# Performance work log

Hardware: AMD Instinct MI355X
Metric: run time of the kernel (lower is better)

Reference implementation:

```python
import jax, jax.numpy as jnp
import numpy as np

B, F, H, D, TE, CE = 16384, 1024, 64, 256, 4, 4

def setup_inputs() -> dict:
    key = jax.random.key(0)
    ks = iter(jax.random.split(key, 40))
    s = 0.02
    mk = lambda shape: jax.random.normal(next(ks), shape, jnp.float32) * s
    inp = {
        'x_A': jax.random.normal(next(ks), (B, F), jnp.float32),
        'x_S': jax.random.normal(next(ks), (B, F), jnp.float32),
        'x_B': jax.random.normal(next(ks), (B, F), jnp.float32),
        # stacked per-expert weights for the three expert groups (A, Shared, B)
        'W1A': mk((TE, F, H)), 'b1A': mk((TE, H)), 'W2A': mk((TE, H, D)), 'b2A': mk((TE, D)),
        'W1S': mk((CE, F, H)), 'b1S': mk((CE, H)), 'W2S': mk((CE, H, D)), 'b2S': mk((CE, D)),
        'W1B': mk((TE, F, H)), 'b1B': mk((TE, H)), 'W2B': mk((TE, H, D)), 'b2B': mk((TE, D)),
        # gate weights
        'WgA': mk((F, TE + CE)), 'bgA': mk((TE + CE,)),
        'WgB': mk((F, TE + CE)), 'bgB': mk((TE + CE,)),
        'WgS': mk((F, 2 * TE + CE)), 'bgS': mk((2 * TE + CE,)),
    }
    return inp

def _expert_group(x, W1, b1, W2, b2):
    # x: [B,F], W1: [E,F,H] -> [B,E,H]; W2: [E,H,D] -> [B,E,D]
    h = jax.nn.relu(jnp.einsum('bf,efh->beh', x, W1) + b1)  # dropout p=0 -> identity
    return jax.nn.relu(jnp.einsum('beh,ehd->bed', h, W2) + b2)

def reference(x_A, x_S, x_B,
              W1A, b1A, W2A, b2A,
              W1S, b1S, W2S, b2S,
              W1B, b1B, W2B, b2B,
              WgA, bgA, WgB, bgB, WgS, bgS):
    EA = _expert_group(x_A, W1A, b1A, W2A, b2A)  # [B,TE,D]
    ES = _expert_group(x_S, W1S, b1S, W2S, b2S)  # [B,CE,D]
    EB = _expert_group(x_B, W1B, b1B, W2B, b2B)  # [B,TE,D]
    gA = jax.nn.softmax(x_A @ WgA + bgA, axis=1)  # [B,TE+CE]
    gS = jax.nn.softmax(x_S @ WgS + bgS, axis=1)  # [B,2TE+CE]
    gB = jax.nn.softmax(x_B @ WgB + bgB, axis=1)  # [B,TE+CE]
    outA = jnp.einsum('bed,be->bd', jnp.concatenate([EA, ES], axis=1), gA)
    outS = jnp.einsum('bed,be->bd', jnp.concatenate([EA, ES, EB], axis=1), gS)
    outB = jnp.einsum('bed,be->bd', jnp.concatenate([EB, ES], axis=1), gB)
    return (outA, outS, outB)
```

## Files before the change

kernel.cpp:

```cpp
#include <hip/hip_runtime.h>


#define BB 16384
#define FF 1024

typedef _Float16 f16;
typedef __fp16 h16x2 __attribute__((ext_vector_type(2)));
typedef _Float16 f16x8 __attribute__((ext_vector_type(8)));
typedef float f32x4 __attribute__((ext_vector_type(4)));

__device__ __forceinline__ void load_lds16(const void* g, void* l) {
    __builtin_amdgcn_global_load_lds(
        (const __attribute__((address_space(1))) unsigned int*)g,
        (__attribute__((address_space(3))) unsigned int*)l, 16, 0, 0);
}

__device__ __forceinline__ f16x8 pack8(float4 lo, float4 hi) {
    union { f16x8 v; h16x2 p[4]; } u;
    u.p[0] = __builtin_amdgcn_cvt_pkrtz(lo.x, lo.y);
    u.p[1] = __builtin_amdgcn_cvt_pkrtz(lo.z, lo.w);
    u.p[2] = __builtin_amdgcn_cvt_pkrtz(hi.x, hi.y);
    u.p[3] = __builtin_amdgcn_cvt_pkrtz(hi.z, hi.w);
    return u.v;
}

__global__ __launch_bounds__(256) void pack_kernel(
    const float* __restrict__ W1A, const float* __restrict__ W1S, const float* __restrict__ W1B,
    const float* __restrict__ W2A, const float* __restrict__ W2S, const float* __restrict__ W2B,
    const float* __restrict__ WgA, const float* __restrict__ WgS, const float* __restrict__ WgB,
    f16* __restrict__ Wp, f16* __restrict__ W2T, f16* __restrict__ Gp)
{
    int idx = blockIdx.x * 256 + threadIdx.x;
    if (idx < 786432) {
        int g = idx / 262144, rem = idx % 262144;
        int c = rem >> 10, k = rem & 1023;
        const float* W1 = (g == 0) ? W1A : ((g == 1) ? W1S : W1B);
        Wp[idx] = (f16)W1[((c >> 6) << 16) + k * 64 + (c & 63)];
    } else if (idx < 983040) {
        int j = idx - 786432;
        int g = j / 65536, rem = j % 65536;
        int e = rem >> 14, rr = rem & 16383;
        int d = rr >> 6, hh = rr & 63;
        const float* W2 = (g == 0) ? W2A : ((g == 1) ? W2S : W2B);
        W2T[j] = (f16)W2[e * 16384 + hh * 256 + d];
    } else {
        int j = idx - 983040;
        int g = j / 16384, rem = j % 16384;
        int c = rem >> 10, k = rem & 1023;
        int ng = (g == 1) ? 12 : 8;
        const float* Wg = (g == 0) ? WgA : ((g == 1) ? WgS : WgB);
        Gp[j] = (c < ng) ? (f16)Wg[k * ng + c] : (f16)0.0f;
    }
}

__global__ __launch_bounds__(512, 2) void fused_kernel(
    const float* __restrict__ xA, const float* __restrict__ xS, const float* __restrict__ xB,
    const float* __restrict__ b1A, const float* __restrict__ b1S, const float* __restrict__ b1B,
    const float* __restrict__ bgA, const float* __restrict__ bgS, const float* __restrict__ bgB,
    const float* __restrict__ b2A, const float* __restrict__ b2S, const float* __restrict__ b2B,
    const f16* __restrict__ Wp,
    const f16* __restrict__ Gp,
    const f16* __restrict__ W2T,
    float* __restrict__ out)
{
    extern __shared__ char smem[];
    f16*   hls   = (f16*)smem;
    char*  stage = smem + 98304;
    float* Xs    = (float*)stage;
    f16*   Ws    = (f16*)(stage + 24576);
    f16*   W2s   = (f16*)stage;
    float* b2s   = (float*)(stage + 32768);
    float* gsh   = (float*)(stage + 45056);
    f16*   Gs    = (f16*)(smem + 157696);

    const int tid  = threadIdx.x;
    const int lane = tid & 63;
    const int w    = tid >> 6;
    const int lrow = lane & 15;
    const int quad = lane >> 4;
    const int row0 = blockIdx.x * 64;

    const int wm = (w >> 2) * 32;
    const int wn = (w & 3) * 64;
    const int rblk = (w & 3) * 16;
    const int wn2  = (w >> 2) * 64;

    const bool gate_wave = ((w & 3) == 0);

    float b1vA[4], b1vS[4], b1vB[4];
#pragma unroll
    for (int j = 0; j < 4; ++j) {
        int c = wn + j * 16 + lrow;
        b1vA[j] = b1A[c]; b1vS[j] = b1S[c]; b1vB[j] = b1B[c];
    }
    float bgv0 = (lrow < 8)  ? bgA[lrow] : 0.0f;
    float bgv1 = (lrow < 12) ? bgS[lrow] : 0.0f;
    float bgv2 = (lrow < 8)  ? bgB[lrow] : 0.0f;

    auto stage_x = [&](int t) {
        int g = t >> 5, k0 = (t & 31) * 32;
        const float* xg = (g == 0) ? xA : ((g == 1) ? xS : xB);
        int s = tid;
        int m = s >> 3, slot = s & 7;
        int seg = slot ^ (m & 7);
        load_lds16(xg + (size_t)(row0 + m) * FF + k0 + seg * 4,
                   Xs + (size_t)(t % 3) * 2048 + s * 4);
    };
    auto stage_w = [&](int t) {
        int g = t >> 5, k0 = (t & 31) * 32;
        const f16* wg = Wp + (size_t)g * 262144;
#pragma unroll
        for (int r = 0; r < 2; ++r) {
            int s = r * 512 + tid;
            int m = s >> 2, slot = s & 3;
            int seg = slot ^ ((m >> 1) & 3);
            load_lds16(wg + (size_t)m * FF + k0 + seg * 8,
                       Ws + (size_t)(t & 1) * 8192 + s * 8);
        }
    };
    auto stage_g = [&](int t) {
        int g = t >> 5, k0 = (t & 31) * 32;
        load_lds16(Gp + (size_t)g * 16384 + (size_t)(lane >> 2) * 1024 + k0 + (lane & 3) * 8,
                   Gs + (size_t)(t & 1) * 512 + lane * 8);
    };

    f32x4 acc[2][4] = {};
    f32x4 gacc[2] = {};
    f32x4 gsvA[2], gsvS[2], gsvB[2];

    auto h_write = [&](int g, const float (&bv)[4]) {
        f16* hb = hls + g * 16384;
#pragma unroll
        for (int j = 0; j < 4; ++j) {
            int col = wn + j * 16 + lrow;
            float bias = bv[j];
#pragma unroll
            for (int i = 0; i < 2; ++i)
#pragma unroll
                for (int r = 0; r < 4; ++r) {
                    int row = wm + i * 16 + quad * 4 + r;
                    float v = fmaxf(acc[i][j][r] + bias, 0.0f);
                    hb[row * 256 + (col ^ ((row & 7) << 3))] = (f16)v;
                }
        }
    };

    stage_x(0);
    __builtin_amdgcn_sched_barrier(0);
    stage_w(0);
    __builtin_amdgcn_sched_barrier(0);
    stage_g(0);
    __builtin_amdgcn_sched_barrier(0);
    stage_x(1);
    __builtin_amdgcn_sched_barrier(0);

    for (int t = 0; t < 96; ++t) {
        int t1 = t + 1;
        int t2 = t + 2;
        if (t < 95) {
            stage_w(t1);
            __builtin_amdgcn_sched_barrier(0);
            stage_g(t1);
            __builtin_amdgcn_sched_barrier(0);
        }
        if (t < 94) {
            stage_x(t2);
            __builtin_amdgcn_sched_barrier(0);
        }
        if (t < 94)      { asm volatile("s_waitcnt vmcnt(5)" ::: "memory"); }
        else if (t == 94){ asm volatile("s_waitcnt vmcnt(4)" ::: "memory"); }
        else             { asm volatile("s_waitcnt vmcnt(0)" ::: "memory"); }
        __builtin_amdgcn_sched_barrier(0);
        __builtin_amdgcn_s_barrier();
        __builtin_amdgcn_sched_barrier(0);

        {
            const float* xb = Xs + (t % 3) * 2048;
            const f16* wb = Ws + (t & 1) * 8192;
            f16x8 af[2], bfr[4];
#pragma unroll
            for (int i = 0; i < 2; ++i) {
                int m = wm + i * 16 + lrow;
                const float* rp = xb + m * 32;
                int s0 = (2 * quad) ^ (m & 7);
                float4 lo = *(const float4*)(rp + s0 * 4);
                float4 hi = *(const float4*)(rp + (s0 ^ 1) * 4);
                af[i] = pack8(lo, hi);
            }
#pragma unroll
            for (int j = 0; j < 4; ++j) {
                int n = wn + j * 16 + lrow;
                int slot = quad ^ ((n >> 1) & 3);
                bfr[j] = *(const f16x8*)(wb + n * 32 + slot * 8);
            }
#pragma unroll
            for (int i = 0; i < 2; ++i)
#pragma unroll
                for (int j = 0; j < 4; ++j)
                    acc[i][j] = __builtin_amdgcn_mfma_f32_16x16x32_f16(af[i], bfr[j], acc[i][j], 0, 0, 0);
            if (gate_wave) {
                f16x8 gb = *(const f16x8*)(Gs + (t & 1) * 512 + lrow * 32 + quad * 8);
#pragma unroll
                for (int i = 0; i < 2; ++i)
                    gacc[i] = __builtin_amdgcn_mfma_f32_16x16x32_f16(af[i], gb, gacc[i], 0, 0, 0);
            }
        }

        if ((t & 31) == 31) {
            int g = t >> 5;
            if (g == 0)      { h_write(0, b1vA); if (gate_wave) { gsvA[0] = gacc[0]; gsvA[1] = gacc[1]; } }
            else if (g == 1) { h_write(1, b1vS); if (gate_wave) { gsvS[0] = gacc[0]; gsvS[1] = gacc[1]; } }
            else             { h_write(2, b1vB); if (gate_wave) { gsvB[0] = gacc[0]; gsvB[1] = gacc[1]; } }
#pragma unroll
            for (int i = 0; i < 2; ++i) {
#pragma unroll
                for (int j = 0; j < 4; ++j) acc[i][j] = (f32x4){0.f, 0.f, 0.f, 0.f};
                gacc[i] = (f32x4){0.f, 0.f, 0.f, 0.f};
            }
        }

        asm volatile("s_waitcnt lgkmcnt(0)" ::: "memory");
        __builtin_amdgcn_sched_barrier(0);
        __builtin_amdgcn_s_barrier();
        __builtin_amdgcn_sched_barrier(0);
    }

    auto stage_w2 = [&](int c, int buf) {
        int p = c >> 1, dh = c & 1;
        int gi = p >> 2, e = p & 3;
        const f16* w2 = W2T + (size_t)(gi * 4 + e) * 16384 + (size_t)dh * 8192;
#pragma unroll
        for (int r = 0; r < 2; ++r) {
            int s = r * 512 + tid;
            int m = s >> 3, slot = s & 7;
            int seg = slot ^ (m & 7);
            load_lds16(w2 + (size_t)m * 64 + seg * 8,
                       W2s + (size_t)buf * 8192 + s * 8);
        }
    };

    {
        const float* s1 = (tid < 256) ? (b2A + tid * 4) : (b2S + (tid - 256) * 4);
        load_lds16(s1, b2s + tid * 4);
        __builtin_amdgcn_sched_barrier(0);
        if (tid < 256) load_lds16(b2B + tid * 4, b2s + 2048 + tid * 4);
        __builtin_amdgcn_sched_barrier(0);
    }
    stage_w2(0, 0);
    __builtin_amdgcn_sched_barrier(0);

    if (gate_wave) {
        auto softmax_store = [&](const f32x4 (&gsv)[2], float bgc, int ng, int goff) {
            int c = lrow;
            bool valid = (c < ng);
#pragma unroll
            for (int i = 0; i < 2; ++i)
#pragma unroll
                for (int r = 0; r < 4; ++r) {
                    int row = wm + i * 16 + quad * 4 + r;
                    float logit = valid ? (gsv[i][r] + bgc) : -1e30f;
                    float mx = logit;
#pragma unroll
                    for (int m = 1; m < 16; m <<= 1) mx = fmaxf(mx, __shfl_xor(mx, m, 16));
                    float ev = valid ? __expf(logit - mx) : 0.0f;
                    float sum = ev;
#pragma unroll
                    for (int m = 1; m < 16; m <<= 1) sum += __shfl_xor(sum, m, 16);
                    if (valid) gsh[row * 28 + goff + c] = ev / sum;
                }
        };
        softmax_store(gsvA, bgv0, 8, 0);
        softmax_store(gsvS, bgv1, 12, 8);
        softmax_store(gsvB, bgv2, 8, 20);
    }
    asm volatile("s_waitcnt vmcnt(2) lgkmcnt(0)" ::: "memory");
    __builtin_amdgcn_sched_barrier(0);
    __builtin_amdgcn_s_barrier();
    __builtin_amdgcn_sched_barrier(0);

    f32x4 oA[2][4] = {}, oS[2][4] = {}, oB[2][4] = {};

    for (int p = 0; p < 12; ++p) {
        int gi = p >> 2, e = p & 3;
#pragma unroll
        for (int dh = 0; dh < 2; ++dh) {
            int c = p * 2 + dh;
            if (c < 23) {
                stage_w2(c + 1, dh ^ 1);
                __builtin_amdgcn_sched_barrier(0);
                asm volatile("s_waitcnt vmcnt(2)" ::: "memory");
            } else {
                asm volatile("s_waitcnt vmcnt(0)" ::: "memory");
            }
            __builtin_amdgcn_sched_barrier(0);
            __builtin_amdgcn_s_barrier();
            __builtin_amdgcn_sched_barrier(0);

            float bias[4];
#pragma unroll
            for (int j = 0; j < 4; ++j)
                bias[j] = b2s[gi * 1024 + e * 256 + dh * 128 + wn2 + j * 16 + lrow];

            const f16* wb = W2s + dh * 8192;
            f32x4 eacc[4] = {};
#pragma unroll
            for (int kk = 0; kk < 2; ++kk) {
                int row = rblk + lrow;
                int u = (kk * 32 + quad * 8) ^ ((row & 7) << 3);
                f16x8 af = *(const f16x8*)(hls + gi * 16384 + row * 256 + e * 64 + u);
                f16x8 bfr[4];
#pragma unroll
                for (int j = 0; j < 4; ++j) {
                    int n = wn2 + j * 16 + lrow;
                    int slot = (kk * 4 + quad) ^ (n & 7);
                    bfr[j] = *(const f16x8*)(wb + n * 64 + slot * 8);
                }
#pragma unroll
                for (int j = 0; j < 4; ++j)
                    eacc[j] = __builtin_amdgcn_mfma_f32_16x16x32_f16(af, bfr[j], eacc[j], 0, 0, 0);
            }

#pragma unroll
            for (int r = 0; r < 4; ++r) {
                int row = rblk + quad * 4 + r;
                float ga = 0.f, gs = 0.f, gb = 0.f;
                if (gi == 0)      { ga = gsh[row * 28 + e];      gs = gsh[row * 28 + 8 + e]; }
                else if (gi == 1) { ga = gsh[row * 28 + 4 + e];  gs = gsh[row * 28 + 12 + e]; gb = gsh[row * 28 + 24 + e]; }
                else              { gs = gsh[row * 28 + 16 + e]; gb = gsh[row * 28 + 20 + e]; }
#pragma unroll
                for (int j = 0; j < 4; ++j) {
                    float v = fmaxf(eacc[j][r] + bias[j], 0.0f);
                    if (gi == 0)      { oA[dh][j][r] += ga * v; oS[dh][j][r] += gs * v; }
                    else if (gi == 1) { oA[dh][j][r] += ga * v; oS[dh][j][r] += gs * v; oB[dh][j][r] += gb * v; }
                    else              { oS[dh][j][r] += gs * v; oB[dh][j][r] += gb * v; }
                }
            }

            asm volatile("s_waitcnt lgkmcnt(0)" ::: "memory");
            __builtin_amdgcn_sched_barrier(0);
            __builtin_amdgcn_s_barrier();
            __builtin_amdgcn_sched_barrier(0);
        }
    }

#pragma unroll
    for (int dh = 0; dh < 2; ++dh)
#pragma unroll
        for (int j = 0; j < 4; ++j) {
            int d = dh * 128 + wn2 + j * 16 + lrow;
#pragma unroll
            for (int r = 0; r < 4; ++r) {
                int row = row0 + rblk + quad * 4 + r;
                out[((size_t)0 * BB + row) * 256 + d] = oA[dh][j][r];
                out[((size_t)1 * BB + row) * 256 + d] = oS[dh][j][r];
                out[((size_t)2 * BB + row) * 256 + d] = oB[dh][j][r];
            }
        }
}

extern "C" void kernel_launch(void* const* d_in, const int* in_sizes, int n_in,
                              void* d_out, int out_size, void* d_ws, size_t ws_size,
                              hipStream_t stream)
{
    (void)in_sizes; (void)n_in; (void)out_size; (void)ws_size;

    const float* xA  = (const float*)d_in[0];
    const float* xS  = (const float*)d_in[1];
    const float* xB  = (const float*)d_in[2];
    const float* W1A = (const float*)d_in[3];
    const float* b1A = (const float*)d_in[4];
    const float* W2A = (const float*)d_in[5];
    const float* b2A = (const float*)d_in[6];
    const float* W1S = (const float*)d_in[7];
    const float* b1S = (const float*)d_in[8];
    const float* W2S = (const float*)d_in[9];
    const float* b2S = (const float*)d_in[10];
    const float* W1B = (const float*)d_in[11];
    const float* b1B = (const float*)d_in[12];
    const float* W2B = (const float*)d_in[13];
    const float* b2B = (const float*)d_in[14];
    const float* WgA = (const float*)d_in[15];
    const float* bgA = (const float*)d_in[16];
    const float* WgB = (const float*)d_in[17];
    const float* bgB = (const float*)d_in[18];
    const float* WgS = (const float*)d_in[19];
    const float* bgS = (const float*)d_in[20];

    char* ws = (char*)d_ws;
    f16* Wp  = (f16*)(ws);
    f16* W2T = (f16*)(ws + 0x180000);
    f16* Gp  = (f16*)(ws + 0x1E0000);

    pack_kernel<<<4032, 256, 0, stream>>>(W1A, W1S, W1B, W2A, W2S, W2B,
                                          WgA, WgS, WgB, Wp, W2T, Gp);
    fused_kernel<<<256, 512, 159744, stream>>>(
        xA, xS, xB, b1A, b1S, b1B, bgA, bgS, bgB, b2A, b2S, b2B,
        Wp, Gp, W2T, (float*)d_out);
}
```

Before: 356.1 us.

## Restructure fused MoE kernel: 32-row blocks, register-streamed weights, tiled transpose pack

The pack kernel now transposes W1 and W2 through shared-memory tiles with vectorized loads and stores instead of one scalar gather per element. The fused kernel moves from 64-row, 512-thread blocks to 32-row, 256-thread blocks with 512 blocks, so grid size doubles and LDS per block roughly halves. Layer-1 and layer-2 weight fragments are loaded straight from global memory into double-buffered registers instead of being staged through LDS. Gate MFMAs now run on every wave, and softmax is done per group inside the main loop. This cuts LDS traffic and barrier work per tile but raises register pressure, and each block now re-reads all weights from global memory or cache.

```diff
diff --git a/kernel.cpp b/kernel.cpp
--- a/kernel.cpp
+++ b/kernel.cpp
@@ -6,6 +6,7 @@
 
 typedef _Float16 f16;
 typedef __fp16 h16x2 __attribute__((ext_vector_type(2)));
+typedef _Float16 f16x4 __attribute__((ext_vector_type(4)));
 typedef _Float16 f16x8 __attribute__((ext_vector_type(8)));
 typedef float f32x4 __attribute__((ext_vector_type(4)));
 
@@ -24,36 +25,82 @@
     return u.v;
 }
 
+#define SBAR() __builtin_amdgcn_sched_barrier(0)
+
 __global__ __launch_bounds__(256) void pack_kernel(
     const float* __restrict__ W1A, const float* __restrict__ W1S, const float* __restrict__ W1B,
     const float* __restrict__ W2A, const float* __restrict__ W2S, const float* __restrict__ W2B,
     const float* __restrict__ WgA, const float* __restrict__ WgS, const float* __restrict__ WgB,
     f16* __restrict__ Wp, f16* __restrict__ W2T, f16* __restrict__ Gp)
 {
-    int idx = blockIdx.x * 256 + threadIdx.x;
-    if (idx < 786432) {
-        int g = idx / 262144, rem = idx % 262144;
-        int c = rem >> 10, k = rem & 1023;
+    __shared__ float T[64 * 65];
+    const int b = blockIdx.x, tid = threadIdx.x;
+
+    if (b < 192) {
+        int g = b >> 6, e = (b >> 4) & 3, k0 = (b & 15) * 64;
         const float* W1 = (g == 0) ? W1A : ((g == 1) ? W1S : W1B);
-        Wp[idx] = (f16)W1[((c >> 6) << 16) + k * 64 + (c & 63)];
-    } else if (idx < 983040) {
-        int j = idx - 786432;
-        int g = j / 65536, rem = j % 65536;
-        int e = rem >> 14, rr = rem & 16383;
-        int d = rr >> 6, hh = rr & 63;
+        const float* src = W1 + e * 65536 + k0 * 64;
+#pragma unroll
+        for (int r = 0; r < 4; ++r) {
+            int slot = r * 256 + tid, kr = slot >> 4, h4 = slot & 15;
+            float4 v = *(const float4*)(src + kr * 64 + h4 * 4);
+            T[(h4 * 4 + 0) * 65 + kr] = v.x;
+            T[(h4 * 4 + 1) * 65 + kr] = v.y;
+            T[(h4 * 4 + 2) * 65 + kr] = v.z;
+            T[(h4 * 4 + 3) * 65 + kr] = v.w;
+        }
+        __syncthreads();
+        f16* dst = Wp + g * 262144 + e * 64 * 1024 + k0;
+#pragma unroll
+        for (int r = 0; r < 4; ++r) {
+            int slot = r * 256 + tid, h = slot >> 4, k4 = slot & 15;
+            f16x4 o;
+            o[0] = (f16)T[h * 65 + k4 * 4 + 0];
+            o[1] = (f16)T[h * 65 + k4 * 4 + 1];
+            o[2] = (f16)T[h * 65 + k4 * 4 + 2];
+            o[3] = (f16)T[h * 65 + k4 * 4 + 3];
+            *(f16x4*)(dst + h * 1024 + k4 * 4) = o;
+        }
+    } else if (b < 240) {
+        int bb = b - 192;
+        int g = bb >> 4, e = (bb >> 2) & 3, d0 = (bb & 3) * 64;
         const float* W2 = (g == 0) ? W2A : ((g == 1) ? W2S : W2B);
-        W2T[j] = (f16)W2[e * 16384 + hh * 256 + d];
+        const float* src = W2 + e * 16384 + d0;
+#pragma unroll
+        for (int r = 0; r < 4; ++r) {
+            int slot = r * 256 + tid, hr = slot >> 4, d4 = slot & 15;
+            float4 v = *(const float4*)(src + hr * 256 + d4 * 4);
+            T[(d4 * 4 + 0) * 65 + hr] = v.x;
+            T[(d4 * 4 + 1) * 65 + hr] = v.y;
+            T[(d4 * 4 + 2) * 65 + hr] = v.z;
+            T[(d4 * 4 + 3) * 65 + hr] = v.w;
+        }
+        __syncthreads();
+        f16* dst = W2T + (g * 4 + e) * 16384 + d0 * 64;
+#pragma unroll
+        for (int r = 0; r < 4; ++r) {
+            int slot = r * 256 + tid, dl = slot >> 4, h4 = slot & 15;
+            f16x4 o;
+            o[0] = (f16)T[dl * 65 + h4 * 4 + 0];
+            o[1] = (f16)T[dl * 65 + h4 * 4 + 1];
+            o[2] = (f16)T[dl * 65 + h4 * 4 + 2];
+            o[3] = (f16)T[dl * 65 + h4 * 4 + 3];
+            *(f16x4*)(dst + dl * 64 + h4 * 4) = o;
+        }
     } else {
-        int j = idx - 983040;
-        int g = j / 16384, rem = j % 16384;
-        int c = rem >> 10, k = rem & 1023;
+        int g = b - 240;
         int ng = (g == 1) ? 12 : 8;
         const float* Wg = (g == 0) ? WgA : ((g == 1) ? WgS : WgB);
-        Gp[j] = (c < ng) ? (f16)Wg[k * ng + c] : (f16)0.0f;
+#pragma unroll 4
+        for (int r = 0; r < 64; ++r) {
+            int idx = r * 256 + tid;
+            int c = idx >> 10, k = idx & 1023;
+            Gp[g * 16384 + idx] = (c < ng) ? (f16)Wg[k * ng + c] : (f16)0.0f;
+        }
     }
 }
 
-__global__ __launch_bounds__(512, 2) void fused_kernel(
+__global__ __launch_bounds__(256, 2) void fused_kernel(
     const float* __restrict__ xA, const float* __restrict__ xS, const float* __restrict__ xB,
     const float* __restrict__ b1A, const float* __restrict__ b1S, const float* __restrict__ b1B,
     const float* __restrict__ bgA, const float* __restrict__ bgS, const float* __restrict__ bgB,
@@ -64,28 +111,18 @@
     float* __restrict__ out)
 {
     extern __shared__ char smem[];
-    f16*   hls   = (f16*)smem;
-    char*  stage = smem + 98304;
-    float* Xs    = (float*)stage;
-    f16*   Ws    = (f16*)(stage + 24576);
-    f16*   W2s   = (f16*)stage;
-    float* b2s   = (float*)(stage + 32768);
-    float* gsh   = (float*)(stage + 45056);
-    f16*   Gs    = (f16*)(smem + 157696);
+    f16*   hls = (f16*)smem;
+    float* Xs  = (float*)(smem + 49152);
+    float* b2s = (float*)(smem + 49152);
+    float* gsh = (float*)(smem + 73728);
 
     const int tid  = threadIdx.x;
     const int lane = tid & 63;
     const int w    = tid >> 6;
     const int lrow = lane & 15;
     const int quad = lane >> 4;
-    const int row0 = blockIdx.x * 64;
-
-    const int wm = (w >> 2) * 32;
-    const int wn = (w & 3) * 64;
-    const int rblk = (w & 3) * 16;
-    const int wn2  = (w >> 2) * 64;
-
-    const bool gate_wave = ((w & 3) == 0);
+    const int row0 = blockIdx.x * 32;
+    const int wn   = w * 64;
 
     float b1vA[4], b1vS[4], b1vB[4];
 #pragma unroll
@@ -97,39 +134,60 @@
     float bgv1 = (lrow < 12) ? bgS[lrow] : 0.0f;
     float bgv2 = (lrow < 8)  ? bgB[lrow] : 0.0f;
 
-    auto stage_x = [&](int t) {
-        int g = t >> 5, k0 = (t & 31) * 32;
+    auto stage_x = [&](int tt) {
+        int g = tt >> 4, kb = (tt & 15) * 64;
         const float* xg = (g == 0) ? xA : ((g == 1) ? xS : xB);
-        int s = tid;
-        int m = s >> 3, slot = s & 7;
-        int seg = slot ^ (m & 7);
-        load_lds16(xg + (size_t)(row0 + m) * FF + k0 + seg * 4,
-                   Xs + (size_t)(t % 3) * 2048 + s * 4);
-    };
-    auto stage_w = [&](int t) {
-        int g = t >> 5, k0 = (t & 31) * 32;
-        const f16* wg = Wp + (size_t)g * 262144;
+        float* dstb = Xs + (tt % 3) * 2048;
 #pragma unroll
         for (int r = 0; r < 2; ++r) {
-            int s = r * 512 + tid;
-            int m = s >> 2, slot = s & 3;
-            int seg = slot ^ ((m >> 1) & 3);
-            load_lds16(wg + (size_t)m * FF + k0 + seg * 8,
-                       Ws + (size_t)(t & 1) * 8192 + s * 8);
-        }
-    };
-    auto stage_g = [&](int t) {
-        int g = t >> 5, k0 = (t & 31) * 32;
-        load_lds16(Gp + (size_t)g * 16384 + (size_t)(lane >> 2) * 1024 + k0 + (lane & 3) * 8,
-                   Gs + (size_t)(t & 1) * 512 + lane * 8);
+            int s = r * 256 + tid;
+            int m = s >> 4, slot = s & 15;
+            int seg = slot ^ (m & 15);
+            load_lds16(xg + (size_t)(row0 + m) * FF + kb + seg * 4, dstb + s * 4);
+        }
+    };
+    auto issue_wf = [&](int tt, f16x8 (&wf)[2][4], f16x8 (&gb)[2]) {
+        int g = tt >> 4, kb = (tt & 15) * 64;
+        const f16* ws = Wp + (size_t)g * 262144;
+        const f16* gs = Gp + (size_t)g * 16384;
+#pragma unroll
+        for (int kk = 0; kk < 2; ++kk) {
+#pragma unroll
+            for (int j = 0; j < 4; ++j)
+                wf[kk][j] = *(const f16x8*)(ws + (size_t)(wn + j * 16 + lrow) * 1024 + kb + kk * 32 + quad * 8);
+            gb[kk] = *(const f16x8*)(gs + (size_t)lrow * 1024 + kb + kk * 32 + quad * 8);
+        }
     };
 
     f32x4 acc[2][4] = {};
     f32x4 gacc[2] = {};
-    f32x4 gsvA[2], gsvS[2], gsvB[2];
+
+    auto compute = [&](int t, f16x8 (&wf)[2][4], f16x8 (&gb)[2]) {
+        const float* xb = Xs + (t % 3) * 2048;
+#pragma unroll
+        for (int kk = 0; kk < 2; ++kk) {
+            f16x8 af[2];
+#pragma unroll
+            for (int i = 0; i < 2; ++i) {
+                int m = i * 16 + lrow;
+                int slot = (kk * 8 + quad * 2) ^ (m & 15);
+                const float* rp = xb + m * 64;
+                float4 lo = *(const float4*)(rp + slot * 4);
+                float4 hi = *(const float4*)(rp + (slot ^ 1) * 4);
+                af[i] = pack8(lo, hi);
+            }
+#pragma unroll
+            for (int i = 0; i < 2; ++i) {
+#pragma unroll
+                for (int j = 0; j < 4; ++j)
+                    acc[i][j] = __builtin_amdgcn_mfma_f32_16x16x32_f16(af[i], wf[kk][j], acc[i][j], 0, 0, 0);
+                gacc[i] = __builtin_amdgcn_mfma_f32_16x16x32_f16(af[i], gb[kk], gacc[i], 0, 0, 0);
+            }
+        }
+    };
 
     auto h_write = [&](int g, const float (&bv)[4]) {
-        f16* hb = hls + g * 16384;
+        f16* hb = hls + g * 8192;
 #pragma unroll
         for (int j = 0; j < 4; ++j) {
             int col = wn + j * 16 + lrow;
@@ -138,224 +196,177 @@
             for (int i = 0; i < 2; ++i)
 #pragma unroll
                 for (int r = 0; r < 4; ++r) {
-                    int row = wm + i * 16 + quad * 4 + r;
+                    int row = i * 16 + quad * 4 + r;
                     float v = fmaxf(acc[i][j][r] + bias, 0.0f);
                     hb[row * 256 + (col ^ ((row & 7) << 3))] = (f16)v;
                 }
         }
-    };
-
-    stage_x(0);
-    __builtin_amdgcn_sched_barrier(0);
-    stage_w(0);
-    __builtin_amdgcn_sched_barrier(0);
-    stage_g(0);
-    __builtin_amdgcn_sched_barrier(0);
-    stage_x(1);
-    __builtin_amdgcn_sched_barrier(0);
-
-    for (int t = 0; t < 96; ++t) {
-        int t1 = t + 1;
-        int t2 = t + 2;
-        if (t < 95) {
-            stage_w(t1);
-            __builtin_amdgcn_sched_barrier(0);
-            stage_g(t1);
-            __builtin_amdgcn_sched_barrier(0);
-        }
-        if (t < 94) {
-            stage_x(t2);
-            __builtin_amdgcn_sched_barrier(0);
-        }
-        if (t < 94)      { asm volatile("s_waitcnt vmcnt(5)" ::: "memory"); }
-        else if (t == 94){ asm volatile("s_waitcnt vmcnt(4)" ::: "memory"); }
-        else             { asm volatile("s_waitcnt vmcnt(0)" ::: "memory"); }
-        __builtin_amdgcn_sched_barrier(0);
+#pragma unroll
+        for (int i = 0; i < 2; ++i)
+#pragma unroll
+            for (int j = 0; j < 4; ++j)
+                acc[i][j] = (f32x4){0.f, 0.f, 0.f, 0.f};
+    };
+
+    auto softmax_store = [&](float bgc, int ng, int goff) {
+        bool valid = (lrow < ng);
+#pragma unroll
+        for (int i = 0; i < 2; ++i)
+#pragma unroll
+            for (int r = 0; r < 4; ++r) {
+                int row = i * 16 + quad * 4 + r;
+                float logit = valid ? (gacc[i][r] + bgc) : -1e30f;
+                float mx = logit;
+#pragma unroll
+                for (int m = 1; m < 16; m <<= 1)
+                    mx = fmaxf(mx, __shfl_xor(mx, m, 16));
+                float ev = valid ? __expf(logit - mx) : 0.0f;
+                float sum = ev;
+#pragma unroll
+                for (int m = 1; m < 16; m <<= 1)
+                    sum += __shfl_xor(sum, m, 16);
+                if (valid) gsh[row * 28 + goff + lrow] = ev / sum;
+            }
+    };
+
+    f16x8 wfA[2][4], gbA[2], wfB[2][4], gbB[2];
+
+    stage_x(0); SBAR();
+    issue_wf(0, wfA, gbA); SBAR();
+    stage_x(1); SBAR();
+
+    auto l1_step = [&](int t, f16x8 (&wfC)[2][4], f16x8 (&gbC)[2],
+                       f16x8 (&wfN)[2][4], f16x8 (&gbN)[2]) {
+        issue_wf(t + 1, wfN, gbN);
+        SBAR();
+        asm volatile("s_waitcnt vmcnt(12) lgkmcnt(0)" ::: "memory");
+        SBAR();
         __builtin_amdgcn_s_barrier();
-        __builtin_amdgcn_sched_barrier(0);
-
-        {
-            const float* xb = Xs + (t % 3) * 2048;
-            const f16* wb = Ws + (t & 1) * 8192;
-            f16x8 af[2], bfr[4];
+        SBAR();
+        stage_x(t + 2);
+        SBAR();
+        compute(t, wfC, gbC);
+    };
+
+    for (int tb = 0; tb < 46; tb += 2) {
+        l1_step(tb, wfA, gbA, wfB, gbB);
+        int t1 = tb + 1;
+        l1_step(t1, wfB, gbB, wfA, gbA);
+        if (t1 == 15) {
+            h_write(0, b1vA);
+            if (w == 0) softmax_store(bgv0, 8, 0);
+#pragma unroll
+            for (int i = 0; i < 2; ++i) gacc[i] = (f32x4){0.f, 0.f, 0.f, 0.f};
+        } else if (t1 == 31) {
+            h_write(1, b1vS);
+            if (w == 0) softmax_store(bgv1, 12, 8);
+#pragma unroll
+            for (int i = 0; i < 2; ++i) gacc[i] = (f32x4){0.f, 0.f, 0.f, 0.f};
+        }
+    }
+
+    f16x8 wf2A[2][4], wf2B[2][4];
+    auto issue_wf2 = [&](int p, f16x8 (&wf)[2][4]) {
+        int gi = p >> 2, e = p & 3;
+        const f16* w2 = W2T + (size_t)(gi * 4 + e) * 16384;
+#pragma unroll
+        for (int kk = 0; kk < 2; ++kk)
+#pragma unroll
+            for (int j = 0; j < 4; ++j)
+                wf[kk][j] = *(const f16x8*)(w2 + (size_t)(wn + j * 16 + lrow) * 64 + kk * 32 + quad * 8);
+    };
+
+    issue_wf(47, wfB, gbB);
+    SBAR();
+    asm volatile("s_waitcnt vmcnt(12) lgkmcnt(0)" ::: "memory");
+    SBAR(); __builtin_amdgcn_s_barrier(); SBAR();
+    compute(46, wfA, gbA);
+
+    asm volatile("s_waitcnt vmcnt(0) lgkmcnt(0)" ::: "memory");
+    SBAR(); __builtin_amdgcn_s_barrier(); SBAR();
+#pragma unroll
+    for (int r = 0; r < 3; ++r) {
+        const float* src = (r == 0) ? (b2A + tid * 4) : ((r == 1) ? (b2S + tid * 4) : (b2B + tid * 4));
+        load_lds16(src, b2s + r * 1024 + tid * 4);
+    }
+    SBAR();
+    issue_wf2(0, wf2A);
+    SBAR();
+    compute(47, wfB, gbB);
+    h_write(2, b1vB);
+    if (w == 0) softmax_store(bgv2, 8, 20);
+
+    asm volatile("s_waitcnt vmcnt(8) lgkmcnt(0)" ::: "memory");
+    SBAR(); __builtin_amdgcn_s_barrier(); SBAR();
+
+    f32x4 oA[2][4] = {}, oS[2][4] = {}, oB[2][4] = {};
+
+    auto l2_pair = [&](int p, f16x8 (&wfC)[2][4], f16x8 (&wfN)[2][4]) {
+        if (p < 11) { issue_wf2(p + 1, wfN); }
+        SBAR();
+        if (p < 11) { asm volatile("s_waitcnt vmcnt(8)" ::: "memory"); }
+        else        { asm volatile("s_waitcnt vmcnt(0)" ::: "memory"); }
+        SBAR();
+        const int gi = p >> 2, e = p & 3;
+        f32x4 eacc[2][4] = {};
+#pragma unroll
+        for (int kk = 0; kk < 2; ++kk) {
+            f16x8 af[2];
 #pragma unroll
             for (int i = 0; i < 2; ++i) {
-                int m = wm + i * 16 + lrow;
-                const float* rp = xb + m * 32;
-                int s0 = (2 * quad) ^ (m & 7);
-                float4 lo = *(const float4*)(rp + s0 * 4);
-                float4 hi = *(const float4*)(rp + (s0 ^ 1) * 4);
-                af[i] = pack8(lo, hi);
+                int m = i * 16 + lrow;
+                int col = (e * 64 + kk * 32 + quad * 8) ^ ((m & 7) << 3);
+                af[i] = *(const f16x8*)(hls + gi * 8192 + m * 256 + col);
             }
 #pragma unroll
-            for (int j = 0; j < 4; ++j) {
-                int n = wn + j * 16 + lrow;
-                int slot = quad ^ ((n >> 1) & 3);
-                bfr[j] = *(const f16x8*)(wb + n * 32 + slot * 8);
+            for (int i = 0; i < 2; ++i)
+#pragma unroll
+                for (int j = 0; j < 4; ++j)
+                    eacc[i][j] = __builtin_amdgcn_mfma_f32_16x16x32_f16(af[i], wfC[kk][j], eacc[i][j], 0, 0, 0);
+        }
+#pragma unroll
+        for (int j = 0; j < 4; ++j) {
+            float bias = b2s[gi * 1024 + e * 256 + wn + j * 16 + lrow];
+#pragma unroll
+            for (int i = 0; i < 2; ++i)
+#pragma unroll
+                for (int r = 0; r < 4; ++r) {
+                    int row = i * 16 + quad * 4 + r;
+                    float v = fmaxf(eacc[i][j][r] + bias, 0.0f);
+                    if (gi == 0) {
+                        oA[i][j][r] += gsh[row * 28 + e] * v;
+                        oS[i][j][r] += gsh[row * 28 + 8 + e] * v;
+                    } else if (gi == 1) {
+                        oA[i][j][r] += gsh[row * 28 + 4 + e] * v;
+                        oS[i][j][r] += gsh[row * 28 + 12 + e] * v;
+                        oB[i][j][r] += gsh[row * 28 + 24 + e] * v;
+                    } else {
+                        oS[i][j][r] += gsh[row * 28 + 16 + e] * v;
+                        oB[i][j][r] += gsh[row * 28 + 20 + e] * v;
+                    }
+                }
+        }
+    };
+
+#pragma unroll
+    for (int pp = 0; pp < 6; ++pp) {
+        l2_pair(2 * pp, wf2A, wf2B);
+        l2_pair(2 * pp + 1, wf2B, wf2A);
+    }
+
+#pragma unroll
+    for (int j = 0; j < 4; ++j) {
+        int d = wn + j * 16 + lrow;
+#pragma unroll
+        for (int i = 0; i < 2; ++i)
+#pragma unroll
+            for (int r = 0; r < 4; ++r) {
+                int row = row0 + i * 16 + quad * 4 + r;
+                out[((size_t)0 * BB + row) * 256 + d] = oA[i][j][r];
+                out[((size_t)1 * BB + row) * 256 + d] = oS[i][j][r];
+                out[((size_t)2 * BB + row) * 256 + d] = oB[i][j][r];
             }
-#pragma unroll
-            for (int i = 0; i < 2; ++i)
-#pragma unroll
-                for (int j = 0; j < 4; ++j)
-                    acc[i][j] = __builtin_amdgcn_mfma_f32_16x16x32_f16(af[i], bfr[j], acc[i][j], 0, 0, 0);
-            if (gate_wave) {
-                f16x8 gb = *(const f16x8*)(Gs + (t & 1) * 512 + lrow * 32 + quad * 8);
-#pragma unroll
-                for (int i = 0; i < 2; ++i)
-                    gacc[i] = __builtin_amdgcn_mfma_f32_16x16x32_f16(af[i], gb, gacc[i], 0, 0, 0);
-            }
-        }
-
-        if ((t & 31) == 31) {
-            int g = t >> 5;
-            if (g == 0)      { h_write(0, b1vA); if (gate_wave) { gsvA[0] = gacc[0]; gsvA[1] = gacc[1]; } }
-            else if (g == 1) { h_write(1, b1vS); if (gate_wave) { gsvS[0] = gacc[0]; gsvS[1] = gacc[1]; } }
-            else             { h_write(2, b1vB); if (gate_wave) { gsvB[0] = gacc[0]; gsvB[1] = gacc[1]; } }
-#pragma unroll
-            for (int i = 0; i < 2; ++i) {
-#pragma unroll
-                for (int j = 0; j < 4; ++j) acc[i][j] = (f32x4){0.f, 0.f, 0.f, 0.f};
-                gacc[i] = (f32x4){0.f, 0.f, 0.f, 0.f};
-            }
-        }
-
-        asm volatile("s_waitcnt lgkmcnt(0)" ::: "memory");
-        __builtin_amdgcn_sched_barrier(0);
-        __builtin_amdgcn_s_barrier();
-        __builtin_amdgcn_sched_barrier(0);
-    }
-
-    auto stage_w2 = [&](int c, int buf) {
-        int p = c >> 1, dh = c & 1;
-        int gi = p >> 2, e = p & 3;
-        const f16* w2 = W2T + (size_t)(gi * 4 + e) * 16384 + (size_t)dh * 8192;
-#pragma unroll
-        for (int r = 0; r < 2; ++r) {
-            int s = r * 512 + tid;
-            int m = s >> 3, slot = s & 7;
-            int seg = slot ^ (m & 7);
-            load_lds16(w2 + (size_t)m * 64 + seg * 8,
-                       W2s + (size_t)buf * 8192 + s * 8);
-        }
-    };
-
-    {
-        const float* s1 = (tid < 256) ? (b2A + tid * 4) : (b2S + (tid - 256) * 4);
-        load_lds16(s1, b2s + tid * 4);
-        __builtin_amdgcn_sched_barrier(0);
-        if (tid < 256) load_lds16(b2B + tid * 4, b2s + 2048 + tid * 4);
-        __builtin_amdgcn_sched_barrier(0);
-    }
-    stage_w2(0, 0);
-    __builtin_amdgcn_sched_barrier(0);
-
-    if (gate_wave) {
-        auto softmax_store = [&](const f32x4 (&gsv)[2], float bgc, int ng, int goff) {
-            int c = lrow;
-            bool valid = (c < ng);
-#pragma unroll
-            for (int i = 0; i < 2; ++i)
-#pragma unroll
-                for (int r = 0; r < 4; ++r) {
-                    int row = wm + i * 16 + quad * 4 + r;
-                    float logit = valid ? (gsv[i][r] + bgc) : -1e30f;
-                    float mx = logit;
-#pragma unroll
-                    for (int m = 1; m < 16; m <<= 1) mx = fmaxf(mx, __shfl_xor(mx, m, 16));
-                    float ev = valid ? __expf(logit - mx) : 0.0f;
-                    float sum = ev;
-#pragma unroll
-                    for (int m = 1; m < 16; m <<= 1) sum += __shfl_xor(sum, m, 16);
-                    if (valid) gsh[row * 28 + goff + c] = ev / sum;
-                }
-        };
-        softmax_store(gsvA, bgv0, 8, 0);
-        softmax_store(gsvS, bgv1, 12, 8);
-        softmax_store(gsvB, bgv2, 8, 20);
-    }
-    asm volatile("s_waitcnt vmcnt(2) lgkmcnt(0)" ::: "memory");
-    __builtin_amdgcn_sched_barrier(0);
-    __builtin_amdgcn_s_barrier();
-    __builtin_amdgcn_sched_barrier(0);
-
-    f32x4 oA[2][4] = {}, oS[2][4] = {}, oB[2][4] = {};
-
-    for (int p = 0; p < 12; ++p) {
-        int gi = p >> 2, e = p & 3;
-#pragma unroll
-        for (int dh = 0; dh < 2; ++dh) {
-            int c = p * 2 + dh;
-            if (c < 23) {
-                stage_w2(c + 1, dh ^ 1);
-                __builtin_amdgcn_sched_barrier(0);
-                asm volatile("s_waitcnt vmcnt(2)" ::: "memory");
-            } else {
-                asm volatile("s_waitcnt vmcnt(0)" ::: "memory");
-            }
-            __builtin_amdgcn_sched_barrier(0);
-            __builtin_amdgcn_s_barrier();
-            __builtin_amdgcn_sched_barrier(0);
-
-            float bias[4];
-#pragma unroll
-            for (int j = 0; j < 4; ++j)
-                bias[j] = b2s[gi * 1024 + e * 256 + dh * 128 + wn2 + j * 16 + lrow];
-
-            const f16* wb = W2s + dh * 8192;
-            f32x4 eacc[4] = {};
-#pragma unroll
-            for (int kk = 0; kk < 2; ++kk) {
-                int row = rblk + lrow;
-                int u = (kk * 32 + quad * 8) ^ ((row & 7) << 3);
-                f16x8 af = *(const f16x8*)(hls + gi * 16384 + row * 256 + e * 64 + u);
-                f16x8 bfr[4];
-#pragma unroll
-                for (int j = 0; j < 4; ++j) {
-                    int n = wn2 + j * 16 + lrow;
-                    int slot = (kk * 4 + quad) ^ (n & 7);
-                    bfr[j] = *(const f16x8*)(wb + n * 64 + slot * 8);
-                }
-#pragma unroll
-                for (int j = 0; j < 4; ++j)
-                    eacc[j] = __builtin_amdgcn_mfma_f32_16x16x32_f16(af, bfr[j], eacc[j], 0, 0, 0);
-            }
-
-#pragma unroll
-            for (int r = 0; r < 4; ++r) {
-                int row = rblk + quad * 4 + r;
-                float ga = 0.f, gs = 0.f, gb = 0.f;
-                if (gi == 0)      { ga = gsh[row * 28 + e];      gs = gsh[row * 28 + 8 + e]; }
-                else if (gi == 1) { ga = gsh[row * 28 + 4 + e];  gs = gsh[row * 28 + 12 + e]; gb = gsh[row * 28 + 24 + e]; }
-                else              { gs = gsh[row * 28 + 16 + e]; gb = gsh[row * 28 + 20 + e]; }
-#pragma unroll
-                for (int j = 0; j < 4; ++j) {
-                    float v = fmaxf(eacc[j][r] + bias[j], 0.0f);
-                    if (gi == 0)      { oA[dh][j][r] += ga * v; oS[dh][j][r] += gs * v; }
-                    else if (gi == 1) { oA[dh][j][r] += ga * v; oS[dh][j][r] += gs * v; oB[dh][j][r] += gb * v; }
-                    else              { oS[dh][j][r] += gs * v; oB[dh][j][r] += gb * v; }
-                }
-            }
-
-            asm volatile("s_waitcnt lgkmcnt(0)" ::: "memory");
-            __builtin_amdgcn_sched_barrier(0);
-            __builtin_amdgcn_s_barrier();
-            __builtin_amdgcn_sched_barrier(0);
-        }
-    }
-
-#pragma unroll
-    for (int dh = 0; dh < 2; ++dh)
-#pragma unroll
-        for (int j = 0; j < 4; ++j) {
-            int d = dh * 128 + wn2 + j * 16 + lrow;
-#pragma unroll
-            for (int r = 0; r < 4; ++r) {
-                int row = row0 + rblk + quad * 4 + r;
-                out[((size_t)0 * BB + row) * 256 + d] = oA[dh][j][r];
-                out[((size_t)1 * BB + row) * 256 + d] = oS[dh][j][r];
-                out[((size_t)2 * BB + row) * 256 + d] = oB[dh][j][r];
-            }
-        }
+    }
 }
 
 extern "C" void kernel_launch(void* const* d_in, const int* in_sizes, int n_in,
@@ -391,9 +402,9 @@
     f16* W2T = (f16*)(ws + 0x180000);
     f16* Gp  = (f16*)(ws + 0x1E0000);
 
-    pack_kernel<<<4032, 256, 0, stream>>>(W1A, W1S, W1B, W2A, W2S, W2B,
-                                          WgA, WgS, WgB, Wp, W2T, Gp);
-    fused_kernel<<<256, 512, 159744, stream>>>(
+    pack_kernel<<<243, 256, 0, stream>>>(W1A, W1S, W1B, W2A, W2S, W2B,
+                                         WgA, WgS, WgB, Wp, W2T, Gp);
+    fused_kernel<<<512, 256, 77312, stream>>>(
         xA, xS, xB, b1A, b1S, b1B, bgA, bgS, bgB, b2A, b2S, b2B,
         Wp, Gp, W2T, (float*)d_out);
 }
```

New measurement: 393.9 us. +10.6%, slower.
